# Optimization experiments

Measured on AMD Instinct MI355X. Metric: run time of the kernel, lower is better.

## Reference

```python
import jax, jax.numpy as jnp
import numpy as np

N_NODES = 50000

def cheb_conv(x, edge_index, W, b):
    # PyG ChebConv, K=2, normalization='sym', lambda_max=2.0 (default):
    # scaled Laplacian L_hat = (2/lambda_max)*L - I = -D^{-1/2} A D^{-1/2} (zero diag).
    # Tx_0 = x, Tx_1 = L_hat @ x ; out = Tx_0 @ W[0] + Tx_1 @ W[1] + b
    src, dst = edge_index[0], edge_index[1]
    ones = jnp.ones(src.shape[0], x.dtype)
    deg = jax.ops.segment_sum(ones, src, num_segments=N_NODES)
    dinv = jnp.where(deg > 0, 1.0 / jnp.sqrt(deg), 0.0)
    norm = -dinv[src] * dinv[dst]                                   # [E]
    tx1 = jax.ops.segment_sum(x[src] * norm[:, None], dst, num_segments=N_NODES)
    return x @ W[0] + tx1 @ W[1] + b

def setup_inputs() -> dict:
    key = jax.random.key(0)
    ks = jax.random.split(key, 12)
    IN, OUT, E, P = 128, 2, 800000, 400000
    return {
        "x": jax.random.normal(ks[0], (N_NODES, IN), jnp.float32),
        "edge_index": jax.random.randint(ks[1], (2, E), 0, N_NODES),
        "E_pos": jax.random.randint(ks[2], (2, P), 0, N_NODES),
        "neg_edge_index": jax.random.randint(ks[3], (2, P), 0, N_NODES),
        "W1": jax.random.normal(ks[4], (2, IN, 300), jnp.float32) * 0.05,
        "b1": jnp.zeros((300,), jnp.float32),
        "W2": jax.random.normal(ks[5], (2, 300, 100), jnp.float32) * 0.05,
        "b2": jnp.zeros((100,), jnp.float32),
        "W3": jax.random.normal(ks[6], (2, 100, OUT), jnp.float32) * 0.05,
        "b3": jnp.zeros((OUT,), jnp.float32),
        "lin1_W": jax.random.normal(ks[7], (100, IN), jnp.float32) * 0.05,
        "lin1_b": jnp.zeros((100,), jnp.float32),
        "lin2_W": jax.random.normal(ks[8], (100, IN), jnp.float32) * 0.05,
        "lin2_b": jnp.zeros((100,), jnp.float32),
        "c1": jnp.full((1,), 0.5, jnp.float32),
        "c2": jnp.full((1,), 0.5, jnp.float32),
    }

def reference(x, edge_index, E_pos, neg_edge_index, W1, b1, W2, b2, W3, b3,
              lin1_W, lin1_b, lin2_W, lin2_b, c1, c2):
    # eval mode: F.dropout and dropout_edge are identity
    x0 = x
    h = jax.nn.relu(cheb_conv(x0, edge_index, W1, b1))
    x1 = jax.nn.relu(cheb_conv(h, edge_index, W2, b2))
    x2 = x1 + jax.nn.relu(x0 @ lin1_W.T + lin1_b)
    z = x1 + jax.nn.relu(x0 @ lin2_W.T + lin2_b)
    pos_score = jnp.sum(z[E_pos[0]] * z[E_pos[1]], axis=1)              # [P]
    pos_loss = -jnp.mean(jnp.log(jax.nn.sigmoid(pos_score) + 1e-15))
    neg_score = jnp.sum(z[neg_edge_index[0]] * z[neg_edge_index[1]], axis=1)
    neg_loss = -jnp.mean(jnp.log(1.0 - jax.nn.sigmoid(neg_score) + 1e-15))
    r_loss = pos_loss + neg_loss
    out = cheb_conv(x2, edge_index, W3, b3)                             # [N, out_channels]
    return (out, r_loss, c1, c2)
```

## Files before the change

### kernel.cpp

```cpp
#include <hip/hip_runtime.h>
#include <math.h>


typedef unsigned short ushort_t;
typedef unsigned char u8;
typedef __attribute__((ext_vector_type(8))) __bf16 bf16x8;
typedef __attribute__((ext_vector_type(8))) short s16x8;
typedef __attribute__((ext_vector_type(4))) float f32x4;
typedef __attribute__((ext_vector_type(2))) float f32x2;

#define NB_H 256
#define HW 12500
#define PW 25000

__device__ __forceinline__ f32x4 mfma16x16x32(s16x8 a, s16x8 b, f32x4 c) {
  return __builtin_amdgcn_mfma_f32_16x16x32_bf16(
      __builtin_bit_cast(bf16x8, a), __builtin_bit_cast(bf16x8, b), c, 0, 0, 0);
}
__device__ __forceinline__ ushort_t f2bf(float f) {
  union { float f; unsigned u; } c; c.f = f;
  unsigned r = (c.u + 0x7FFFu + ((c.u >> 16) & 1u)) >> 16;
  return (ushort_t)r;
}
__device__ __forceinline__ f32x2 cvt2lo(unsigned u) {
  return __builtin_amdgcn_cvt_pk_f32_fp8((int)u, false);
}
__device__ __forceinline__ f32x2 cvt2hi(unsigned u) {
  return __builtin_amdgcn_cvt_pk_f32_fp8((int)u, true);
}
__device__ __forceinline__ u8 f2fp8(float f) {
  return (u8)(__builtin_amdgcn_cvt_pk_fp8_f32(f, 0.f, 0, false) & 0xff);
}

template<int VAR, int NT, int KTOT>
__global__ __launch_bounds__(256) void gemm_mfma(
    const ushort_t* __restrict__ A0, const ushort_t* __restrict__ A1,
    const ushort_t* __restrict__ Wt,
    const float* __restrict__ bias0, const float* __restrict__ bias1,
    const float* __restrict__ x1,
    const float* __restrict__ W3c, const float* __restrict__ b3c,
    void* __restrict__ out0, void* __restrict__ out1,
    float* __restrict__ t0g, float* __restrict__ t1g, int M)
{
  constexpr int NF = NT / 32;
  __shared__ __align__(16) ushort_t As[64 * 40];
  __shared__ __align__(16) ushort_t Bs[NT * 40];
  __shared__ float w3s[400];
  const int tid  = threadIdx.x;
  const int lane = tid & 63, w = tid >> 6;
  const int m0 = blockIdx.x * 64;
  const int wm = (w & 1) * 32, wn = (w >> 1) * (NT / 2);
  if (VAR == 2) { for (int i = tid; i < 400; i += 256) w3s[i] = W3c[i]; }
  f32x4 acc[2][NF];
#pragma unroll
  for (int i = 0; i < 2; ++i)
#pragma unroll
    for (int j = 0; j < NF; ++j) acc[i][j] = (f32x4){0.f, 0.f, 0.f, 0.f};

  for (int k0 = 0; k0 < KTOT; k0 += 32) {
    {
      const int r = tid >> 2, c8 = (tid & 3) * 8;
      const int gm = m0 + r;
      uint4 v = {0u, 0u, 0u, 0u};
      if (gm < M) {
        const ushort_t* srcp;
        if (VAR == 0) srcp = (k0 < 128) ? A0 + (size_t)gm * 128 + k0 + c8
                                        : A1 + (size_t)gm * 128 + (k0 - 128) + c8;
        else if (VAR == 1) srcp = A0 + (size_t)gm * 320 + k0 + c8;
        else srcp = A0 + (size_t)gm * 128 + k0 + c8;
        v = *(const uint4*)srcp;
      }
      *(uint4*)&As[r * 40 + c8] = v;
    }
    {
      const int c8 = (tid & 3) * 8;
#pragma unroll
      for (int i = 0; i < (NT * 4 + 255) / 256; ++i) {
        const int r = (tid >> 2) + i * 64;
        if (r < NT)
          *(uint4*)&Bs[r * 40 + c8] = *(const uint4*)(Wt + (size_t)r * KTOT + k0 + c8);
      }
    }
    __syncthreads();
    s16x8 af[2], bfr[NF];
#pragma unroll
    for (int mi = 0; mi < 2; ++mi)
      af[mi] = *(const s16x8*)&As[(wm + mi * 16 + (lane & 15)) * 40 + (lane >> 4) * 8];
#pragma unroll
    for (int ni = 0; ni < NF; ++ni)
      bfr[ni] = *(const s16x8*)&Bs[(wn + ni * 16 + (lane & 15)) * 40 + (lane >> 4) * 8];
#pragma unroll
    for (int mi = 0; mi < 2; ++mi)
#pragma unroll
      for (int ni = 0; ni < NF; ++ni)
        acc[mi][ni] = mfma16x16x32(af[mi], bfr[ni], acc[mi][ni]);
    __syncthreads();
  }

  if (VAR == 2) {
#pragma unroll
    for (int mi = 0; mi < 2; ++mi)
#pragma unroll
      for (int r = 0; r < 4; ++r) {
        const int gRow = m0 + wm + mi * 16 + ((lane >> 4) << 2) + r;
        float p0 = 0.f, p1 = 0.f, p2 = 0.f, p3 = 0.f;
#pragma unroll
        for (int ni = 0; ni < NF; ++ni) {
          const int col = wn + ni * 16 + (lane & 15);
          const float v = acc[mi][ni][r];
          if (gRow < M) {
            if (col < 100) {
              const float x2v = x1[(size_t)gRow * 128 + col] + fmaxf(v + bias0[col], 0.f);
              p0 = fmaf(x2v, w3s[col * 2 + 0], p0);
              p1 = fmaf(x2v, w3s[col * 2 + 1], p1);
              p2 = fmaf(x2v, w3s[200 + col * 2 + 0], p2);
              p3 = fmaf(x2v, w3s[200 + col * 2 + 1], p3);
            } else if (col < 200) {
              const int c = col - 100;
              ((u8*)out1)[(size_t)gRow * 128 + c] =
                  f2fp8(x1[(size_t)gRow * 128 + c] + fmaxf(v + bias1[c], 0.f));
            }
          }
        }
        if (wn == 0) {
#pragma unroll
          for (int off = 8; off; off >>= 1) {
            p0 += __shfl_down(p0, off, 16);
            p1 += __shfl_down(p1, off, 16);
            p2 += __shfl_down(p2, off, 16);
            p3 += __shfl_down(p3, off, 16);
          }
          if ((lane & 15) == 0 && gRow < M) {
            t0g[(size_t)gRow * 2 + 0] = p0 + b3c[0];
            t0g[(size_t)gRow * 2 + 1] = p1 + b3c[1];
            t1g[(size_t)gRow * 2 + 0] = p2;
            t1g[(size_t)gRow * 2 + 1] = p3;
          }
        }
      }
  } else {
#pragma unroll
    for (int mi = 0; mi < 2; ++mi)
#pragma unroll
      for (int ni = 0; ni < NF; ++ni)
#pragma unroll
        for (int r = 0; r < 4; ++r) {
          const int gRow = m0 + wm + mi * 16 + ((lane >> 4) << 2) + r;
          const int col  = wn + ni * 16 + (lane & 15);
          if (gRow >= M) continue;
          const float v = acc[mi][ni][r];
          if (VAR == 0) {
            ushort_t* h = (ushort_t*)out0;
            h[(size_t)gRow * 320 + col] = (col < 300) ? f2bf(fmaxf(v + bias0[col], 0.f))
                                                      : (ushort_t)0;
          } else {
            if (col < 100) ((float*)out0)[(size_t)gRow * 128 + col] = v + bias0[col];
            else if (col < 200) ((u8*)out1)[(size_t)gRow * 128 + (col - 100)] = f2fp8(v);
          }
        }
  }
}

__global__ void cvt_x_kernel(const float* __restrict__ x, ushort_t* __restrict__ xb,
                             u8* __restrict__ xf8, int n4) {
  const int i = blockIdx.x * 256 + threadIdx.x;
  if (i < n4) {
    const float4 v = ((const float4*)x)[i];
    ushort4 o; o.x = f2bf(v.x); o.y = f2bf(v.y); o.z = f2bf(v.z); o.w = f2bf(v.w);
    ((ushort4*)xb)[i] = o;
    int p = 0;
    p = __builtin_amdgcn_cvt_pk_fp8_f32(v.x, v.y, p, false);
    p = __builtin_amdgcn_cvt_pk_fp8_f32(v.z, v.w, p, true);
    ((unsigned*)xf8)[i] = (unsigned)p;
  }
}
__global__ void pack_all(const float* __restrict__ W1, const float* __restrict__ W2,
                         const float* __restrict__ l1W, const float* __restrict__ l2W,
                         ushort_t* __restrict__ W1t, ushort_t* __restrict__ W2t,
                         ushort_t* __restrict__ Wlt) {
  const int i = blockIdx.x * 256 + threadIdx.x;
  if (i < 81920) {
    const int n = i >> 8, k = i & 255;
    float v = 0.f;
    if (n < 300) v = (k < 128) ? W1[k * 300 + n] : W1[38400 + (k - 128) * 300 + n];
    W1t[i] = f2bf(v);
  } else if (i < 153600) {
    const int j = i - 81920;
    const int n = j / 320, k = j - n * 320;
    float v = 0.f;
    if (n < 200 && k < 300) v = W2[(n < 100 ? 0 : 30000) + k * 100 + (n % 100)];
    W2t[j] = f2bf(v);
  } else if (i < 182272) {
    const int j = i - 153600;
    const int n = j >> 7, k = j & 127;
    float v = 0.f;
    if (n < 100) v = l1W[n * 128 + k];
    else if (n < 200) v = l2W[(n - 100) * 128 + k];
    Wlt[j] = f2bf(v);
  }
}

__global__ __launch_bounds__(256) void hist2(
    const int* __restrict__ src, const int* __restrict__ dst, int E, int M,
    unsigned* __restrict__ partS, unsigned* __restrict__ partD,
    ushort_t* __restrict__ rank)
{
  __shared__ unsigned hist[HW];
  const int b = blockIdx.x;
  const int cs = (E + NB_H - 1) / NB_H;
  const int e0 = b * cs;
  const int e1 = (e0 + cs < E) ? e0 + cs : E;
  for (int isD = 0; isD < 2; ++isD) {
    const int* keys = isD ? dst : src;
    unsigned* part = isD ? partD : partS;
    for (int r = 0; r < 2; ++r) {
      const int klo = r * 2 * HW;
      for (int i = threadIdx.x; i < HW; i += 256) hist[i] = 0;
      __syncthreads();
      for (int e = e0 + threadIdx.x; e < e1; e += 256) {
        const int k = keys[e] - klo;
        if ((unsigned)k < (unsigned)(2 * HW)) {
          const unsigned old = atomicAdd(&hist[k >> 1], (k & 1) ? 0x10000u : 1u);
          if (isD) rank[e] = (ushort_t)((old >> ((k & 1) * 16)) & 0xffffu);
        }
      }
      __syncthreads();
      for (int i = threadIdx.x; i < HW; i += 256)
        part[(size_t)b * PW + r * HW + i] = hist[i];
      __syncthreads();
    }
  }
}

__global__ void reduce_base(const unsigned* __restrict__ partS,
                            unsigned* __restrict__ partD,
                            float* __restrict__ dinv, int* __restrict__ cnt, int M)
{
  const int i = blockIdx.x * 256 + threadIdx.x;
  if (i >= PW) return;
  unsigned s0 = 0, s1 = 0;
  for (int b = 0; b < NB_H; ++b) {
    const unsigned v = partS[(size_t)b * PW + i];
    s0 += v & 0xffffu; s1 += v >> 16;
  }
  unsigned r0 = 0, r1 = 0;
  for (int b = 0; b < NB_H; ++b) {
    const unsigned v = partD[(size_t)b * PW + i];
    partD[(size_t)b * PW + i] = r0 | (r1 << 16);
    r0 += v & 0xffffu; r1 += v >> 16;
  }
  const int k = 2 * i;
  if (k < M) {
    dinv[k] = s0 ? 1.f / sqrtf((float)s0) : 0.f;
    cnt[k] = (int)r0;
  }
  if (k + 1 < M) {
    dinv[k + 1] = s1 ? 1.f / sqrtf((float)s1) : 0.f;
    cnt[k + 1] = (int)r1;
  }
}

__global__ void scan_local(const int* __restrict__ cnt, int* __restrict__ ptr,
                           int* __restrict__ bsum, int n)
{
  __shared__ int tmp[256];
  const int i = blockIdx.x * 256 + threadIdx.x;
  const int v = (i < n) ? cnt[i] : 0;
  tmp[threadIdx.x] = v;
  __syncthreads();
  for (int off = 1; off < 256; off <<= 1) {
    const int t = (threadIdx.x >= off) ? tmp[threadIdx.x - off] : 0;
    __syncthreads();
    tmp[threadIdx.x] += t;
    __syncthreads();
  }
  if (i < n) ptr[i] = tmp[threadIdx.x] - v;
  if (threadIdx.x == 255) bsum[blockIdx.x] = tmp[255];
}
__global__ void scan_bsum(int* __restrict__ bsum, int nb) {
  __shared__ int tmp[256];
  const int v = (threadIdx.x < nb) ? bsum[threadIdx.x] : 0;
  tmp[threadIdx.x] = v;
  __syncthreads();
  for (int off = 1; off < 256; off <<= 1) {
    const int t = (threadIdx.x >= off) ? tmp[threadIdx.x - off] : 0;
    __syncthreads();
    tmp[threadIdx.x] += t;
    __syncthreads();
  }
  if (threadIdx.x < nb) bsum[threadIdx.x] = tmp[threadIdx.x] - v;
}
__global__ void scan_add(int* __restrict__ ptr, const int* __restrict__ bsum, int n, int E) {
  const int i = blockIdx.x * 256 + threadIdx.x;
  if (i < n) ptr[i] += bsum[blockIdx.x];
  if (i == 0) ptr[n] = E;
}

__global__ void fill_csr2(const int* __restrict__ src, const int* __restrict__ dst,
                          const float* __restrict__ dinv, const int* __restrict__ ptr,
                          const unsigned* __restrict__ base32,
                          const ushort_t* __restrict__ rank,
                          int2* __restrict__ csr, int E)
{
  const int e = blockIdx.x * 256 + threadIdx.x;
  if (e >= E) return;
  const int cs = (E + NB_H - 1) / NB_H;
  const int b = e / cs;
  const int s = src[e], d = dst[e];
  const unsigned bv = base32[(size_t)b * PW + (d >> 1)];
  const int base = (int)((bv >> ((d & 1) * 16)) & 0xffffu);
  const int pos = ptr[d] + base + (int)rank[e];
  const float w = -dinv[s] * dinv[d];
  csr[pos] = make_int2(s, __float_as_int(w));
}

#define ACCV(u, ww) { f32x2 t; \
  t = cvt2lo(u.x); a[0]  = fmaf(ww, t.x, a[0]);  a[1]  = fmaf(ww, t.y, a[1]);  \
  t = cvt2hi(u.x); a[2]  = fmaf(ww, t.x, a[2]);  a[3]  = fmaf(ww, t.y, a[3]);  \
  t = cvt2lo(u.y); a[4]  = fmaf(ww, t.x, a[4]);  a[5]  = fmaf(ww, t.y, a[5]);  \
  t = cvt2hi(u.y); a[6]  = fmaf(ww, t.x, a[6]);  a[7]  = fmaf(ww, t.y, a[7]);  \
  t = cvt2lo(u.z); a[8]  = fmaf(ww, t.x, a[8]);  a[9]  = fmaf(ww, t.y, a[9]);  \
  t = cvt2hi(u.z); a[10] = fmaf(ww, t.x, a[10]); a[11] = fmaf(ww, t.y, a[11]); \
  t = cvt2lo(u.w); a[12] = fmaf(ww, t.x, a[12]); a[13] = fmaf(ww, t.y, a[13]); \
  t = cvt2hi(u.w); a[14] = fmaf(ww, t.x, a[14]); a[15] = fmaf(ww, t.y, a[15]); }

__global__ __launch_bounds__(256) void gather128e(
    const u8* __restrict__ xf8, ushort_t* __restrict__ txb,
    const int* __restrict__ ptr, const int2* __restrict__ csr, int M)
{
  const int node = (blockIdx.x * 256 + threadIdx.x) >> 3;
  const int sub  = threadIdx.x & 7;
  if (node >= M) return;
  const int beg = ptr[node], end = ptr[node + 1];
  float a[16] = {};
  int p = beg;
  for (; p + 4 <= end; p += 4) {
    const int2 e0 = csr[p], e1 = csr[p + 1], e2 = csr[p + 2], e3 = csr[p + 3];
    const float w0 = __int_as_float(e0.y), w1 = __int_as_float(e1.y);
    const float w2 = __int_as_float(e2.y), w3 = __int_as_float(e3.y);
    const uint4 v0 = *(const uint4*)(xf8 + (size_t)e0.x * 128 + sub * 16);
    const uint4 v1 = *(const uint4*)(xf8 + (size_t)e1.x * 128 + sub * 16);
    const uint4 v2 = *(const uint4*)(xf8 + (size_t)e2.x * 128 + sub * 16);
    const uint4 v3 = *(const uint4*)(xf8 + (size_t)e3.x * 128 + sub * 16);
    ACCV(v0, w0) ACCV(v1, w1) ACCV(v2, w2) ACCV(v3, w3)
  }
  for (; p < end; ++p) {
    const int2 eq = csr[p]; const float wq = __int_as_float(eq.y);
    const uint4 v = *(const uint4*)(xf8 + (size_t)eq.x * 128 + sub * 16);
    ACCV(v, wq)
  }
  uint4 o1, o2;
  o1.x = (unsigned)f2bf(a[0])  | ((unsigned)f2bf(a[1])  << 16);
  o1.y = (unsigned)f2bf(a[2])  | ((unsigned)f2bf(a[3])  << 16);
  o1.z = (unsigned)f2bf(a[4])  | ((unsigned)f2bf(a[5])  << 16);
  o1.w = (unsigned)f2bf(a[6])  | ((unsigned)f2bf(a[7])  << 16);
  o2.x = (unsigned)f2bf(a[8])  | ((unsigned)f2bf(a[9])  << 16);
  o2.y = (unsigned)f2bf(a[10]) | ((unsigned)f2bf(a[11]) << 16);
  o2.z = (unsigned)f2bf(a[12]) | ((unsigned)f2bf(a[13]) << 16);
  o2.w = (unsigned)f2bf(a[14]) | ((unsigned)f2bf(a[15]) << 16);
  ushort_t* dstp = txb + (size_t)node * 128 + sub * 16;
  *(uint4*)dstp = o1;
  *(uint4*)(dstp + 8) = o2;
}

__global__ __launch_bounds__(256) void gather100e_x1(
    const u8* __restrict__ Brh, float* __restrict__ Ar,
    const int* __restrict__ ptr, const int2* __restrict__ csr, int M)
{
  const int node = (blockIdx.x * 256 + threadIdx.x) >> 3;
  const int sub  = threadIdx.x & 7;
  if (node >= M) return;
  const int beg = ptr[node], end = ptr[node + 1];
  float a[16] = {};
  int p = beg;
  for (; p + 4 <= end; p += 4) {
    const int2 e0 = csr[p], e1 = csr[p + 1], e2 = csr[p + 2], e3 = csr[p + 3];
    const float w0 = __int_as_float(e0.y), w1 = __int_as_float(e1.y);
    const float w2 = __int_as_float(e2.y), w3 = __int_as_float(e3.y);
    const uint4 v0 = *(const uint4*)(Brh + (size_t)e0.x * 128 + sub * 16);
    const uint4 v1 = *(const uint4*)(Brh + (size_t)e1.x * 128 + sub * 16);
    const uint4 v2 = *(const uint4*)(Brh + (size_t)e2.x * 128 + sub * 16);
    const uint4 v3 = *(const uint4*)(Brh + (size_t)e3.x * 128 + sub * 16);
    ACCV(v0, w0) ACCV(v1, w1) ACCV(v2, w2) ACCV(v3, w3)
  }
  for (; p < end; ++p) {
    const int2 eq = csr[p]; const float wq = __int_as_float(eq.y);
    const uint4 v = *(const uint4*)(Brh + (size_t)eq.x * 128 + sub * 16);
    ACCV(v, wq)
  }
  float* dstp = Ar + (size_t)node * 128 + sub * 16;
#pragma unroll
  for (int q = 0; q < 4; ++q) {
    float4 b = *(const float4*)(dstp + q * 4);
    b.x = fmaxf(b.x + a[q * 4 + 0], 0.f);
    b.y = fmaxf(b.y + a[q * 4 + 1], 0.f);
    b.z = fmaxf(b.z + a[q * 4 + 2], 0.f);
    b.w = fmaxf(b.w + a[q * 4 + 3], 0.f);
    *(float4*)(dstp + q * 4) = b;
  }
}
#undef ACCV

#define DOTV(uu, vv, s) { f32x2 p_, q_; \
  p_ = cvt2lo(uu.x); q_ = cvt2lo(vv.x); s = fmaf(p_.x, q_.x, s); s = fmaf(p_.y, q_.y, s); \
  p_ = cvt2hi(uu.x); q_ = cvt2hi(vv.x); s = fmaf(p_.x, q_.x, s); s = fmaf(p_.y, q_.y, s); \
  p_ = cvt2lo(uu.y); q_ = cvt2lo(vv.y); s = fmaf(p_.x, q_.x, s); s = fmaf(p_.y, q_.y, s); \
  p_ = cvt2hi(uu.y); q_ = cvt2hi(vv.y); s = fmaf(p_.x, q_.x, s); s = fmaf(p_.y, q_.y, s); \
  p_ = cvt2lo(uu.z); q_ = cvt2lo(vv.z); s = fmaf(p_.x, q_.x, s); s = fmaf(p_.y, q_.y, s); \
  p_ = cvt2hi(uu.z); q_ = cvt2hi(vv.z); s = fmaf(p_.x, q_.x, s); s = fmaf(p_.y, q_.y, s); \
  p_ = cvt2lo(uu.w); q_ = cvt2lo(vv.w); s = fmaf(p_.x, q_.x, s); s = fmaf(p_.y, q_.y, s); \
  p_ = cvt2hi(uu.w); q_ = cvt2hi(vv.w); s = fmaf(p_.x, q_.x, s); s = fmaf(p_.y, q_.y, s); }

__global__ __launch_bounds__(256) void loss_fp8(
    const u8* __restrict__ zf8, const int* __restrict__ ep,
    const int* __restrict__ en, int P, float* __restrict__ acc)
{
  __shared__ float red[8];
  const int tid = threadIdx.x;
  const int lane = tid & 63, wib = tid >> 6;
  const int sub = tid & 7;
  const int slot0 = blockIdx.x * 32 + (tid >> 3);
  const int step = gridDim.x * 32;
  float tp = 0.f, tn = 0.f;
  int g = slot0;
  for (; g + step < 2 * P; g += 2 * step) {
    const int gA = g, gB = g + step;
    const int negA = (gA >= P), negB = (gB >= P);
    const int pA = negA ? gA - P : gA, pB = negB ? gB - P : gB;
    const int* iA = negA ? en : ep;
    const int* iB = negB ? en : ep;
    const int naA = iA[pA], nbA = iA[P + pA];
    const int naB = iB[pB], nbB = iB[P + pB];
    const uint4 ra1 = *(const uint4*)(zf8 + (size_t)naA * 128 + sub * 16);
    const uint4 rb1 = *(const uint4*)(zf8 + (size_t)nbA * 128 + sub * 16);
    const uint4 ra2 = *(const uint4*)(zf8 + (size_t)naB * 128 + sub * 16);
    const uint4 rb2 = *(const uint4*)(zf8 + (size_t)nbB * 128 + sub * 16);
    float sA = 0.f, sB = 0.f;
    DOTV(ra1, rb1, sA)
    DOTV(ra2, rb2, sB)
#pragma unroll
    for (int off = 4; off; off >>= 1) {
      sA += __shfl_down(sA, off, 8);
      sB += __shfl_down(sB, off, 8);
    }
    if (sub == 0) {
      const float gA_ = 1.f / (1.f + expf(-sA));
      if (negA) tn += logf(1.f - gA_ + 1e-15f); else tp += logf(gA_ + 1e-15f);
      const float gB_ = 1.f / (1.f + expf(-sB));
      if (negB) tn += logf(1.f - gB_ + 1e-15f); else tp += logf(gB_ + 1e-15f);
    }
  }
  if (g < 2 * P) {
    const int neg = (g >= P);
    const int p = neg ? g - P : g;
    const int* ia = neg ? en : ep;
    const int na = ia[p], nb = ia[P + p];
    const uint4 ra = *(const uint4*)(zf8 + (size_t)na * 128 + sub * 16);
    const uint4 rb = *(const uint4*)(zf8 + (size_t)nb * 128 + sub * 16);
    float s = 0.f;
    DOTV(ra, rb, s)
#pragma unroll
    for (int off = 4; off; off >>= 1) s += __shfl_down(s, off, 8);
    if (sub == 0) {
      const float sig = 1.f / (1.f + expf(-s));
      if (neg) tn += logf(1.f - sig + 1e-15f); else tp += logf(sig + 1e-15f);
    }
  }
  tp += __shfl_down(tp, 32, 64); tn += __shfl_down(tn, 32, 64);
  tp += __shfl_down(tp, 16, 64); tn += __shfl_down(tn, 16, 64);
  tp += __shfl_down(tp, 8, 64);  tn += __shfl_down(tn, 8, 64);
  if (lane == 0) { red[wib] = tp; red[4 + wib] = tn; }
  __syncthreads();
  if (tid == 0) {
    atomicAdd(acc + 0, red[0] + red[1] + red[2] + red[3]);
    atomicAdd(acc + 1, red[4] + red[5] + red[6] + red[7]);
  }
}
#undef DOTV

__global__ void gather2_final(
    const float* __restrict__ t1, const float* __restrict__ t0,
    const int* __restrict__ ptr, const int2* __restrict__ csr,
    const float* __restrict__ accs,
    const float* __restrict__ c1, const float* __restrict__ c2,
    float* __restrict__ out, int M, float invP)
{
  const int i = blockIdx.x * blockDim.x + threadIdx.x;
  if (i < M) {
    float a0 = 0.f, a1 = 0.f;
    const int beg = ptr[i], end = ptr[i + 1];
    int p = beg;
    for (; p + 4 <= end; p += 4) {
      const int2 e0 = csr[p], e1 = csr[p + 1], e2 = csr[p + 2], e3 = csr[p + 3];
      const float w0 = __int_as_float(e0.y), w1 = __int_as_float(e1.y);
      const float w2 = __int_as_float(e2.y), w3 = __int_as_float(e3.y);
      const float2 v0 = *(const float2*)(t1 + (size_t)e0.x * 2);
      const float2 v1 = *(const float2*)(t1 + (size_t)e1.x * 2);
      const float2 v2 = *(const float2*)(t1 + (size_t)e2.x * 2);
      const float2 v3 = *(const float2*)(t1 + (size_t)e3.x * 2);
      a0 = fmaf(w0, v0.x, a0); a1 = fmaf(w0, v0.y, a1);
      a0 = fmaf(w1, v1.x, a0); a1 = fmaf(w1, v1.y, a1);
      a0 = fmaf(w2, v2.x, a0); a1 = fmaf(w2, v2.y, a1);
      a0 = fmaf(w3, v3.x, a0); a1 = fmaf(w3, v3.y, a1);
    }
    for (; p < end; ++p) {
      const int2 eq = csr[p]; const float wq = __int_as_float(eq.y);
      const float2 v = *(const float2*)(t1 + (size_t)eq.x * 2);
      a0 = fmaf(wq, v.x, a0); a1 = fmaf(wq, v.y, a1);
    }
    const float2 base = *(const float2*)(t0 + (size_t)i * 2);
    *(float2*)(out + (size_t)i * 2) = make_float2(base.x + a0, base.y + a1);
  }
  if (i == 0) {
    out[2 * M + 0] = -(accs[0] + accs[1]) * invP;
    out[2 * M + 1] = c1[0];
    out[2 * M + 2] = c2[0];
  }
}

extern "C" void kernel_launch(void* const* d_in, const int* in_sizes, int n_in,
                              void* d_out, int out_size, void* d_ws, size_t ws_size,
                              hipStream_t stream)
{
  const float* x   = (const float*)d_in[0];
  const int*   ei  = (const int*)d_in[1];
  const int*   ep  = (const int*)d_in[2];
  const int*   en  = (const int*)d_in[3];
  const float* W1  = (const float*)d_in[4];
  const float* b1  = (const float*)d_in[5];
  const float* W2  = (const float*)d_in[6];
  const float* b2  = (const float*)d_in[7];
  const float* W3  = (const float*)d_in[8];
  const float* b3  = (const float*)d_in[9];
  const float* l1W = (const float*)d_in[10];
  const float* l1b = (const float*)d_in[11];
  const float* l2W = (const float*)d_in[12];
  const float* l2b = (const float*)d_in[13];
  const float* c1  = (const float*)d_in[14];
  const float* c2  = (const float*)d_in[15];
  float* out = (float*)d_out;

  const int M = in_sizes[0] / 128;
  const int E = in_sizes[1] / 2;
  const int P = in_sizes[2] / 2;
  const int* src = ei;
  const int* dst = ei + E;
  const int nb_scan = (M + 255) / 256;

  float* ws = (float*)d_ws;
  size_t o = 0;
  float*    dinv = ws + o;            o += 50176;
  int*      cnt  = (int*)(ws + o);    o += (size_t)M;
  int*      ptr  = (int*)(ws + o);    o += (size_t)M + 8;
  int*      bsum = (int*)(ws + o);    o += 256;
  int2*     csr  = (int2*)(ws + o);   o += (size_t)E * 2;
  ushort_t* rank = (ushort_t*)(ws + o); o += (size_t)E / 2;
  ushort_t* xb   = (ushort_t*)(ws + o); o += (size_t)M * 64;
  u8*       xf8  = (u8*)(ws + o);     o += (size_t)M * 32;
  ushort_t* tx0b = (ushort_t*)(ws + o); o += (size_t)M * 64;
  ushort_t* W1t  = (ushort_t*)(ws + o); o += 40960;
  ushort_t* W2t  = (ushort_t*)(ws + o); o += 35840;
  ushort_t* Wlt  = (ushort_t*)(ws + o); o += 14336;
  ushort_t* h    = (ushort_t*)(ws + o); o += (size_t)M * 160;
  float*    Ar   = ws + o;            o += (size_t)M * 128;
  u8*       Brh  = (u8*)(ws + o);     o += (size_t)M * 32;
  u8*       zf8  = (u8*)(ws + o);     o += (size_t)M * 32;
  float*    t0   = ws + o;            o += (size_t)M * 2;
  float*    t1   = ws + o;            o += (size_t)M * 2;
  float*    accs = ws + o;            o += 8;
  unsigned* partS = (unsigned*)h;
  unsigned* partD = (unsigned*)Ar;

  hipMemsetAsync(accs, 0, 2 * 4, stream);
  hipMemsetAsync(Brh,  0, (size_t)M * 128, stream);
  hipMemsetAsync(zf8,  0, (size_t)M * 128, stream);

  cvt_x_kernel<<<(M * 32 + 255) / 256, 256, 0, stream>>>(x, xb, xf8, M * 32);
  pack_all<<<(182272 + 255) / 256, 256, 0, stream>>>(W1, W2, l1W, l2W, W1t, W2t, Wlt);

  hist2<<<NB_H, 256, 0, stream>>>(src, dst, E, M, partS, partD, rank);
  reduce_base<<<(PW + 255) / 256, 256, 0, stream>>>(partS, partD, dinv, cnt, M);
  scan_local<<<nb_scan, 256, 0, stream>>>(cnt, ptr, bsum, M);
  scan_bsum<<<1, 256, 0, stream>>>(bsum, nb_scan);
  scan_add<<<nb_scan, 256, 0, stream>>>(ptr, bsum, M, E);
  fill_csr2<<<(E + 255) / 256, 256, 0, stream>>>(src, dst, dinv, ptr, partD, rank, csr, E);

  const int gB = (M + 63) / 64;
  const int gE8 = (M * 8 + 255) / 256;

  gather128e<<<gE8, 256, 0, stream>>>(xf8, tx0b, ptr, csr, M);
  gemm_mfma<0, 320, 256><<<gB, 256, 0, stream>>>(
      xb, tx0b, W1t, b1, nullptr, nullptr, nullptr, nullptr, h, nullptr, nullptr, nullptr, M);

  gemm_mfma<1, 224, 320><<<gB, 256, 0, stream>>>(
      h, nullptr, W2t, b2, nullptr, nullptr, nullptr, nullptr, Ar, Brh, nullptr, nullptr, M);
  gather100e_x1<<<gE8, 256, 0, stream>>>(Brh, Ar, ptr, csr, M);

  gemm_mfma<2, 224, 128><<<gB, 256, 0, stream>>>(
      xb, nullptr, Wlt, l1b, l2b, Ar , W3, b3, nullptr, zf8, t0, t1, M);

  loss_fp8<<<2048, 256, 0, stream>>>(zf8, ep, en, P, accs);

  gather2_final<<<(M + 255) / 256, 256, 0, stream>>>(t1, t0, ptr, csr,
                                                     accs, c1, c2, out, M, 1.0f / (float)P);
}
```

Measured before the change: 483.8 us.

## Parallelize histogram reduce across 8 lanes and deepen gather/score load batching

The histogram base reduction now splits the 256 partial blocks across 8 lanes per bin pair, with a segmented shuffle scan to build the exclusive prefix. This replaces the serial 256-deep loop that ran on only about 25k threads. The two CSR gather kernels unroll to 8 in-flight edges instead of 4, and the link-score kernel processes 4 pairs per iteration instead of 2, to raise memory-level parallelism. In exchange it uses more registers per thread, which may lower occupancy.

New measurement: 481.5 us. No clear change (-0.5%).

```diff
diff --git a/kernel.cpp b/kernel.cpp
--- a/kernel.cpp
+++ b/kernel.cpp
@@ -232,31 +232,42 @@
   }
 }
 
-__global__ void reduce_base(const unsigned* __restrict__ partS,
-                            unsigned* __restrict__ partD,
-                            float* __restrict__ dinv, int* __restrict__ cnt, int M)
-{
-  const int i = blockIdx.x * 256 + threadIdx.x;
+__global__ __launch_bounds__(256) void reduce_base8(
+    const unsigned* __restrict__ partS, unsigned* __restrict__ partD,
+    float* __restrict__ dinv, int* __restrict__ cnt, int M)
+{
+  const int gtid = blockIdx.x * 256 + threadIdx.x;
+  const int i = gtid >> 3;
+  const int t = gtid & 7;
   if (i >= PW) return;
-  unsigned s0 = 0, s1 = 0;
-  for (int b = 0; b < NB_H; ++b) {
-    const unsigned v = partS[(size_t)b * PW + i];
-    s0 += v & 0xffffu; s1 += v >> 16;
-  }
-  unsigned r0 = 0, r1 = 0;
-  for (int b = 0; b < NB_H; ++b) {
-    const unsigned v = partD[(size_t)b * PW + i];
-    partD[(size_t)b * PW + i] = r0 | (r1 << 16);
-    r0 += v & 0xffffu; r1 += v >> 16;
-  }
-  const int k = 2 * i;
-  if (k < M) {
-    dinv[k] = s0 ? 1.f / sqrtf((float)s0) : 0.f;
-    cnt[k] = (int)r0;
-  }
-  if (k + 1 < M) {
-    dinv[k + 1] = s1 ? 1.f / sqrtf((float)s1) : 0.f;
-    cnt[k + 1] = (int)r1;
+  const int b0 = t * 32;
+  unsigned ssum = 0;
+#pragma unroll 8
+  for (int b = 0; b < 32; ++b) ssum += partS[(size_t)(b0 + b) * PW + i];
+#pragma unroll
+  for (int off = 4; off; off >>= 1) ssum += __shfl_down(ssum, off, 8);
+  unsigned vals[32];
+#pragma unroll 8
+  for (int b = 0; b < 32; ++b) vals[b] = partD[(size_t)(b0 + b) * PW + i];
+  unsigned run = 0;
+#pragma unroll
+  for (int b = 0; b < 32; ++b) { const unsigned v = vals[b]; vals[b] = run; run += v; }
+  unsigned inc = run;
+#pragma unroll
+  for (int off = 1; off < 8; off <<= 1) {
+    const unsigned u = __shfl_up(inc, off, 8);
+    if (t >= off) inc += u;
+  }
+  const unsigned excl = inc - run;
+  const unsigned total = __shfl(inc, 7, 8);
+#pragma unroll 8
+  for (int b = 0; b < 32; ++b) partD[(size_t)(b0 + b) * PW + i] = vals[b] + excl;
+  if (t == 0) {
+    const int k = 2 * i;
+    const unsigned s0 = ssum & 0xffffu, s1 = ssum >> 16;
+    const unsigned d0 = total & 0xffffu, d1 = total >> 16;
+    if (k < M) { dinv[k] = s0 ? 1.f / sqrtf((float)s0) : 0.f; cnt[k] = (int)d0; }
+    if (k + 1 < M) { dinv[k + 1] = s1 ? 1.f / sqrtf((float)s1) : 0.f; cnt[k + 1] = (int)d1; }
   }
 }
 
@@ -334,15 +345,16 @@
   const int beg = ptr[node], end = ptr[node + 1];
   float a[16] = {};
   int p = beg;
-  for (; p + 4 <= end; p += 4) {
-    const int2 e0 = csr[p], e1 = csr[p + 1], e2 = csr[p + 2], e3 = csr[p + 3];
-    const float w0 = __int_as_float(e0.y), w1 = __int_as_float(e1.y);
-    const float w2 = __int_as_float(e2.y), w3 = __int_as_float(e3.y);
-    const uint4 v0 = *(const uint4*)(xf8 + (size_t)e0.x * 128 + sub * 16);
-    const uint4 v1 = *(const uint4*)(xf8 + (size_t)e1.x * 128 + sub * 16);
-    const uint4 v2 = *(const uint4*)(xf8 + (size_t)e2.x * 128 + sub * 16);
-    const uint4 v3 = *(const uint4*)(xf8 + (size_t)e3.x * 128 + sub * 16);
-    ACCV(v0, w0) ACCV(v1, w1) ACCV(v2, w2) ACCV(v3, w3)
+  for (; p + 8 <= end; p += 8) {
+    int2 e[8];
+#pragma unroll
+    for (int q = 0; q < 8; ++q) e[q] = csr[p + q];
+    uint4 v[8];
+#pragma unroll
+    for (int q = 0; q < 8; ++q)
+      v[q] = *(const uint4*)(xf8 + (size_t)e[q].x * 128 + sub * 16);
+#pragma unroll
+    for (int q = 0; q < 8; ++q) { const float wq = __int_as_float(e[q].y); ACCV(v[q], wq) }
   }
   for (; p < end; ++p) {
     const int2 eq = csr[p]; const float wq = __int_as_float(eq.y);
@@ -373,15 +385,16 @@
   const int beg = ptr[node], end = ptr[node + 1];
   float a[16] = {};
   int p = beg;
-  for (; p + 4 <= end; p += 4) {
-    const int2 e0 = csr[p], e1 = csr[p + 1], e2 = csr[p + 2], e3 = csr[p + 3];
-    const float w0 = __int_as_float(e0.y), w1 = __int_as_float(e1.y);
-    const float w2 = __int_as_float(e2.y), w3 = __int_as_float(e3.y);
-    const uint4 v0 = *(const uint4*)(Brh + (size_t)e0.x * 128 + sub * 16);
-    const uint4 v1 = *(const uint4*)(Brh + (size_t)e1.x * 128 + sub * 16);
-    const uint4 v2 = *(const uint4*)(Brh + (size_t)e2.x * 128 + sub * 16);
-    const uint4 v3 = *(const uint4*)(Brh + (size_t)e3.x * 128 + sub * 16);
-    ACCV(v0, w0) ACCV(v1, w1) ACCV(v2, w2) ACCV(v3, w3)
+  for (; p + 8 <= end; p += 8) {
+    int2 e[8];
+#pragma unroll
+    for (int q = 0; q < 8; ++q) e[q] = csr[p + q];
+    uint4 v[8];
+#pragma unroll
+    for (int q = 0; q < 8; ++q)
+      v[q] = *(const uint4*)(Brh + (size_t)e[q].x * 128 + sub * 16);
+#pragma unroll
+    for (int q = 0; q < 8; ++q) { const float wq = __int_as_float(e[q].y); ACCV(v[q], wq) }
   }
   for (; p < end; ++p) {
     const int2 eq = csr[p]; const float wq = __int_as_float(eq.y);
@@ -423,34 +436,39 @@
   const int step = gridDim.x * 32;
   float tp = 0.f, tn = 0.f;
   int g = slot0;
-  for (; g + step < 2 * P; g += 2 * step) {
-    const int gA = g, gB = g + step;
-    const int negA = (gA >= P), negB = (gB >= P);
-    const int pA = negA ? gA - P : gA, pB = negB ? gB - P : gB;
-    const int* iA = negA ? en : ep;
-    const int* iB = negB ? en : ep;
-    const int naA = iA[pA], nbA = iA[P + pA];
-    const int naB = iB[pB], nbB = iB[P + pB];
-    const uint4 ra1 = *(const uint4*)(zf8 + (size_t)naA * 128 + sub * 16);
-    const uint4 rb1 = *(const uint4*)(zf8 + (size_t)nbA * 128 + sub * 16);
-    const uint4 ra2 = *(const uint4*)(zf8 + (size_t)naB * 128 + sub * 16);
-    const uint4 rb2 = *(const uint4*)(zf8 + (size_t)nbB * 128 + sub * 16);
-    float sA = 0.f, sB = 0.f;
-    DOTV(ra1, rb1, sA)
-    DOTV(ra2, rb2, sB)
+  for (; g + 3 * step < 2 * P; g += 4 * step) {
+    int neg[4], na[4], nb[4];
+#pragma unroll
+    for (int q = 0; q < 4; ++q) {
+      const int gq = g + q * step;
+      neg[q] = (gq >= P);
+      const int p = neg[q] ? gq - P : gq;
+      const int* ia = neg[q] ? en : ep;
+      na[q] = ia[p]; nb[q] = ia[P + p];
+    }
+    uint4 ra[4], rb[4];
+#pragma unroll
+    for (int q = 0; q < 4; ++q) {
+      ra[q] = *(const uint4*)(zf8 + (size_t)na[q] * 128 + sub * 16);
+      rb[q] = *(const uint4*)(zf8 + (size_t)nb[q] * 128 + sub * 16);
+    }
+    float s[4] = {0.f, 0.f, 0.f, 0.f};
+#pragma unroll
+    for (int q = 0; q < 4; ++q) DOTV(ra[q], rb[q], s[q])
 #pragma unroll
     for (int off = 4; off; off >>= 1) {
-      sA += __shfl_down(sA, off, 8);
-      sB += __shfl_down(sB, off, 8);
+#pragma unroll
+      for (int q = 0; q < 4; ++q) s[q] += __shfl_down(s[q], off, 8);
     }
     if (sub == 0) {
-      const float gA_ = 1.f / (1.f + expf(-sA));
-      if (negA) tn += logf(1.f - gA_ + 1e-15f); else tp += logf(gA_ + 1e-15f);
-      const float gB_ = 1.f / (1.f + expf(-sB));
-      if (negB) tn += logf(1.f - gB_ + 1e-15f); else tp += logf(gB_ + 1e-15f);
-    }
-  }
-  if (g < 2 * P) {
+#pragma unroll
+      for (int q = 0; q < 4; ++q) {
+        const float sig = 1.f / (1.f + expf(-s[q]));
+        if (neg[q]) tn += logf(1.f - sig + 1e-15f); else tp += logf(sig + 1e-15f);
+      }
+    }
+  }
+  for (; g < 2 * P; g += step) {
     const int neg = (g >= P);
     const int p = neg ? g - P : g;
     const int* ia = neg ? en : ep;
@@ -579,7 +597,7 @@
   pack_all<<<(182272 + 255) / 256, 256, 0, stream>>>(W1, W2, l1W, l2W, W1t, W2t, Wlt);
 
   hist2<<<NB_H, 256, 0, stream>>>(src, dst, E, M, partS, partD, rank);
-  reduce_base<<<(PW + 255) / 256, 256, 0, stream>>>(partS, partD, dinv, cnt, M);
+  reduce_base8<<<(PW * 8 + 255) / 256, 256, 0, stream>>>(partS, partD, dinv, cnt, M);
   scan_local<<<nb_scan, 256, 0, stream>>>(cnt, ptr, bsum, M);
   scan_bsum<<<1, 256, 0, stream>>>(bsum, nb_scan);
   scan_add<<<nb_scan, 256, 0, stream>>>(ptr, bsum, M, E);
```
